# Optimization experiments

Measured on AMD Instinct MI355X. Metric: run time of the kernel, lower is better.

## Reference

```python
import jax, jax.numpy as jnp
import numpy as np

NEG_SLOPE = 0.2

def gat_conv(x, edge_index, W, a_src, a_dst, bias, heads, channels):
    # PyG GATConv (add_self_loops=False, dropout off in eval)
    N = x.shape[0]
    h = (x @ W).reshape(N, heads, channels)               # [N,H,C]
    src, dst = edge_index[0], edge_index[1]
    e_src = jnp.einsum('nhc,hc->nh', h, a_src)            # [N,H]
    e_dst = jnp.einsum('nhc,hc->nh', h, a_dst)
    e = jax.nn.leaky_relu(e_src[src] + e_dst[dst], NEG_SLOPE)  # [E,H]
    # softmax over incoming edges of each destination node
    m = jax.ops.segment_max(e, dst, num_segments=N)       # [N,H]
    ex = jnp.exp(e - m[dst])
    s = jax.ops.segment_sum(ex, dst, num_segments=N)
    alpha = ex / (s[dst] + 1e-16)                         # [E,H]
    msg = h[src] * alpha[:, :, None]                      # [E,H,C]
    out = jax.ops.segment_sum(msg, dst, num_segments=N)   # [N,H,C]
    return out.reshape(N, heads * channels) + bias


def setup_inputs() -> dict:
    key = jax.random.key(0)
    ks = jax.random.split(key, 12)
    N, E, SED, HID, H, F_OUT = 20000, 320000, 768, 128, 4, 128
    return {
        'x': jax.random.normal(ks[0], (N, SED), jnp.float32),
        'edge_index': jax.random.randint(ks[1], (2, E), 0, N, jnp.int32),
        'sentence_embedding': jax.random.normal(ks[2], (SED,), jnp.float32),
        'W1': jax.random.normal(ks[3], (2 * SED, H * HID), jnp.float32) * 0.02,
        'a1_src': jax.random.normal(ks[4], (H, HID), jnp.float32) * 0.1,
        'a1_dst': jax.random.normal(ks[5], (H, HID), jnp.float32) * 0.1,
        'b1': jax.random.normal(ks[6], (H * HID,), jnp.float32) * 0.02,
        'W2': jax.random.normal(ks[7], (H * HID, F_OUT), jnp.float32) * 0.02,
        'a2_src': jax.random.normal(ks[8], (1, F_OUT), jnp.float32) * 0.1,
        'a2_dst': jax.random.normal(ks[9], (1, F_OUT), jnp.float32) * 0.1,
        'b2': jax.random.normal(ks[10], (F_OUT,), jnp.float32) * 0.02,
    }


def reference(x, edge_index, sentence_embedding, W1, a1_src, a1_dst, b1, W2, a2_src, a2_dst, b2):
    N = x.shape[0]
    sent = jnp.broadcast_to(sentence_embedding[None, :], (N, sentence_embedding.shape[0]))
    h = jnp.concatenate([x, sent], axis=1)                # [N, 2*SED]
    h = gat_conv(h, edge_index, W1, a1_src, a1_dst, b1, heads=4, channels=128)
    h = jax.nn.elu(h)
    out = gat_conv(h, edge_index, W2, a2_src, a2_dst, b2, heads=1, channels=128)
    return out
```

## Files before the change

### kernel.cpp

```cpp
#include <hip/hip_runtime.h>
#include <cstdint>
#include <cstddef>

#define NSLOPE 0.2f

typedef __attribute__((ext_vector_type(8))) short bf16x8;
typedef __attribute__((ext_vector_type(4))) float f32x4;
typedef __attribute__((ext_vector_type(2))) float f32x2;
typedef unsigned short ushort_t;

__device__ inline ushort_t f2bf(float f) {
    union { float f; unsigned u; } v; v.f = f;
    unsigned u = v.u;
    unsigned r = (u + 0x7fffu + ((u >> 16) & 1u)) >> 16;
    return (ushort_t)r;
}
__device__ inline float bf2f(ushort_t u) {
    union { unsigned u; float f; } v; v.u = ((unsigned)u) << 16;
    return v.f;
}
__device__ inline float2 unpack_bf2(unsigned u) {
    return make_float2(bf2f((ushort_t)(u & 0xffffu)), bf2f((ushort_t)(u >> 16)));
}
__device__ inline f32x2 unpack2(unsigned u) {
    union { unsigned u; float f; } lo, hi;
    lo.u = u << 16;
    hi.u = u & 0xffff0000u;
    f32x2 r; r.x = lo.f; r.y = hi.f;
    return r;
}
__device__ inline float leaky(float v) { return (v > 0.f) ? v : NSLOPE * v; }
__device__ inline float sel4(float4 q, bool b1, bool b2) {
    return b2 ? (b1 ? q.w : q.z) : (b1 ? q.y : q.x);
}

__global__ __launch_bounds__(256) void prep_kernel(
    const float* __restrict__ x, ushort_t* __restrict__ x_bf16, size_t nx,
    const float* __restrict__ W1, ushort_t* __restrict__ W1T,
    const float* __restrict__ W2, ushort_t* __restrict__ W2T,
    const float* __restrict__ sent, float* __restrict__ svec_part,
    int* __restrict__ indeg, int N, int nbCast, int nbZero)
{
    __shared__ float tile[32][33];
    int bid = blockIdx.x;
    int tid = threadIdx.x;
    if (bid < nbCast) {
        size_t i = ((size_t)bid * 256 + tid) * 8;
        if (i < nx) {
            float4 v0 = *(const float4*)(x + i);
            float4 v1 = *(const float4*)(x + i + 4);
            ushort_t r[8] = { f2bf(v0.x), f2bf(v0.y), f2bf(v0.z), f2bf(v0.w),
                              f2bf(v1.x), f2bf(v1.y), f2bf(v1.z), f2bf(v1.w) };
            *(uint4*)(x_bf16 + i) = *(uint4*)r;
        }
        return;
    }
    bid -= nbCast;
    if (bid < 384) {
        int k0 = (bid % 24) * 32, n0 = (bid / 24) * 32;
        int tx = tid & 31, ty = tid >> 5;
#pragma unroll
        for (int i = 0; i < 4; ++i)
            tile[ty + i * 8][tx] = W1[(size_t)(k0 + ty + i * 8) * 512 + n0 + tx];
        __syncthreads();
#pragma unroll
        for (int i = 0; i < 4; ++i)
            W1T[(size_t)(n0 + ty + i * 8) * 768 + k0 + tx] = f2bf(tile[tx][ty + i * 8]);
        return;
    }
    bid -= 384;
    if (bid < 64) {
        int k0 = (bid % 16) * 32, n0 = (bid / 16) * 32;
        int tx = tid & 31, ty = tid >> 5;
#pragma unroll
        for (int i = 0; i < 4; ++i)
            tile[ty + i * 8][tx] = W2[(size_t)(k0 + ty + i * 8) * 128 + n0 + tx];
        __syncthreads();
#pragma unroll
        for (int i = 0; i < 4; ++i)
            W2T[(size_t)(n0 + ty + i * 8) * 512 + k0 + tx] = f2bf(tile[tx][ty + i * 8]);
        return;
    }
    bid -= 64;
    if (bid < 16) {
        int cb = bid & 1, kb = bid >> 1;
        int c = cb * 256 + tid;
        int k0 = kb * 96;
        float acc = 0.f;
#pragma unroll 8
        for (int k = k0; k < k0 + 96; ++k)
            acc += sent[k] * W1[(size_t)(768 + k) * 512 + c];
        svec_part[kb * 512 + c] = acc;
        return;
    }
    bid -= 16;
    {
        int i = bid * 256 + tid;
        if (i < N) indeg[i] = 0;
    }
}

__device__ inline void async_copy16(const void* g, void* l) {
    __builtin_amdgcn_global_load_lds(
        (const __attribute__((address_space(1))) unsigned int*)g,
        (__attribute__((address_space(3))) unsigned int*)l, 16, 0, 0);
}

__global__ __launch_bounds__(256) void mfma_gemm_kernel(
    const ushort_t* __restrict__ A,
    const ushort_t* __restrict__ BT,
    const float* __restrict__ bias,
    ushort_t* __restrict__ Cb,
    const float* __restrict__ asrc,
    const float* __restrict__ adst,
    float* __restrict__ e_src,
    float* __restrict__ e_dst,
    int eStride,
    int M, int K, int Nc)
{
    __shared__ __align__(16) ushort_t lA[2][128 * 32];
    __shared__ __align__(16) ushort_t lB[2][128 * 32];
    __shared__ float e_lds[128][2][2];
    const int tid = threadIdx.x;
    const int wave = tid >> 6;
    const int lane = tid & 63;
    const int col0 = blockIdx.x * 128;
    const int row0 = blockIdx.y * 128;
    const int wm = (wave & 1) * 64;
    const int wn = (wave >> 1) * 64;
    const int q = lane >> 4;
    const int ml = lane & 15;

    f32x4 acc[4][4] = {};

    int rowS[2], gS[2];
#pragma unroll
    for (int i = 0; i < 2; ++i) {
        int p = wave * 128 + i * 64 + lane;
        int r = p >> 2, s = p & 3;
        rowS[i] = r;
        gS[i] = s ^ ((r >> 1) & 3);
    }

    auto stage = [&](int k0, int buf) {
#pragma unroll
        for (int i = 0; i < 2; ++i) {
            int pb = wave * 128 + i * 64;
            int r = rowS[i];
            int ga = min(row0 + r, M - 1);
            async_copy16(A + (size_t)ga * K + k0 + gS[i] * 8, &lA[buf][(size_t)pb * 8]);
            async_copy16(BT + (size_t)(col0 + r) * K + k0 + gS[i] * 8, &lB[buf][(size_t)pb * 8]);
        }
    };

    stage(0, 0);
    __syncthreads();
    int pb = 0;
    for (int k0 = 0; k0 < K; k0 += 32) {
        if (k0 + 32 < K) stage(k0 + 32, pb ^ 1);
        bf16x8 af[4], bfr[4];
#pragma unroll
        for (int t = 0; t < 4; ++t) {
            int m = wm + t * 16 + ml;
            af[t] = *(const bf16x8*)&lA[pb][(size_t)(m * 4 + (q ^ ((m >> 1) & 3))) * 8];
            int n = wn + t * 16 + ml;
            bfr[t] = *(const bf16x8*)&lB[pb][(size_t)(n * 4 + (q ^ ((n >> 1) & 3))) * 8];
        }
#pragma unroll
        for (int tm = 0; tm < 4; ++tm)
#pragma unroll
            for (int tn = 0; tn < 4; ++tn)
                acc[tm][tn] = __builtin_amdgcn_mfma_f32_16x16x32_bf16(
                    af[tm], bfr[tn], acc[tm][tn], 0, 0, 0);
        __syncthreads();
        pb ^= 1;
    }

    float es_acc[4][4] = {};
    float ed_acc[4][4] = {};
#pragma unroll
    for (int tm = 0; tm < 4; ++tm) {
        int rbase = row0 + wm + tm * 16 + q * 4;
#pragma unroll
        for (int tn = 0; tn < 4; ++tn) {
            int col = col0 + wn + tn * 16 + ml;
            float bb = bias ? bias[col] : 0.f;
            float av = asrc[col];
            float dv = adst[col];
#pragma unroll
            for (int r = 0; r < 4; ++r) {
                int row = rbase + r;
                float val = acc[tm][tn][r] + bb;
                if (row < M)
                    Cb[(size_t)row * Nc + col] = f2bf(val);
                es_acc[tm][r] += val * av;
                ed_acc[tm][r] += val * dv;
            }
        }
    }
    const int colhalf = wave >> 1;
#pragma unroll
    for (int tm = 0; tm < 4; ++tm) {
#pragma unroll
        for (int r = 0; r < 4; ++r) {
            float es = es_acc[tm][r], ed2 = ed_acc[tm][r];
#pragma unroll
            for (int st = 1; st < 16; st <<= 1) {
                es += __shfl_xor(es, st);
                ed2 += __shfl_xor(ed2, st);
            }
            if (ml == 0) {
                int rl = wm + tm * 16 + q * 4 + r;
                e_lds[rl][colhalf][0] = es;
                e_lds[rl][colhalf][1] = ed2;
            }
        }
    }
    __syncthreads();
    if (tid < 128) {
        int row = row0 + tid;
        if (row < M) {
            float es = e_lds[tid][0][0] + e_lds[tid][1][0];
            float ed2 = e_lds[tid][0][1] + e_lds[tid][1][1];
            e_src[(size_t)row * eStride + blockIdx.x] = es;
            e_dst[(size_t)row * eStride + blockIdx.x] = ed2;
        }
    }
}

__global__ void count_kernel(const int* __restrict__ ei, int* __restrict__ indeg, int E) {
    int e = blockIdx.x * blockDim.x + threadIdx.x;
    if (e < E) atomicAdd(&indeg[ei[E + e]], 1);
}

__global__ __launch_bounds__(1024) void scan_kernel(const int* __restrict__ indeg,
                                                    int* __restrict__ offsets,
                                                    int* __restrict__ cursor,
                                                    const float* __restrict__ svec_part,
                                                    float* __restrict__ svec, int N) {
    __shared__ int partial[1024];
    int tid = threadIdx.x;
    if (tid < 512) {
        float s = 0.f;
#pragma unroll
        for (int kb = 0; kb < 8; ++kb) s += svec_part[kb * 512 + tid];
        svec[tid] = s;
    }
    int per = (N + 1023) / 1024;
    int start = tid * per;
    int end = min(start + per, N);
    int sum = 0;
    if (start + per <= N && (per & 3) == 0) {
        for (int i = 0; i < per; i += 4) {
            int4 v = *(const int4*)(indeg + start + i);
            sum += v.x + v.y + v.z + v.w;
        }
    } else {
        for (int i = start; i < end; ++i) sum += indeg[i];
    }
    partial[tid] = sum;
    __syncthreads();
    for (int st = 1; st < 1024; st <<= 1) {
        int v = (tid >= st) ? partial[tid - st] : 0;
        __syncthreads();
        partial[tid] += v;
        __syncthreads();
    }
    int run = (tid == 0) ? 0 : partial[tid - 1];
    if (start + per <= N && (per & 3) == 0) {
        for (int i = 0; i < per; i += 4) {
            int4 v = *(const int4*)(indeg + start + i);
            int4 o;
            o.x = run;
            o.y = o.x + v.x;
            o.z = o.y + v.y;
            o.w = o.z + v.z;
            run = o.w + v.w;
            *(int4*)(offsets + start + i) = o;
            *(int4*)(cursor + start + i) = o;
        }
    } else {
        for (int i = start; i < end; ++i) {
            offsets[i] = run; cursor[i] = run;
            run += indeg[i];
        }
    }
    if (tid == 1023) offsets[N] = run;
}

__global__ void scatter_kernel(const int* __restrict__ ei, int* __restrict__ cursor,
                               int* __restrict__ csr_src, int E) {
    int e = blockIdx.x * blockDim.x + threadIdx.x;
    if (e < E) {
        int d = ei[E + e];
        int p = atomicAdd(&cursor[d], 1);
        csr_src[p] = ei[e];
    }
}

__global__ __launch_bounds__(256) void gather1_kernel(
    const ushort_t* __restrict__ h1b, const float* __restrict__ e_src,
    const float* __restrict__ e_dst, const int* __restrict__ offsets,
    const int* __restrict__ csr_src, const float* __restrict__ bias,
    ushort_t* __restrict__ outb, int N)
{
    int node = __builtin_amdgcn_readfirstlane(blockIdx.x * 4 + (threadIdx.x >> 6));
    int lane = threadIdx.x & 63;
    if (node >= N) return;
    int beg = offsets[node], end = offsets[node + 1];
    float4 ed = *(const float4*)&e_dst[node * 4];

    float m[4] = { -1e30f, -1e30f, -1e30f, -1e30f };
    float s[4] = { 0.f, 0.f, 0.f, 0.f };
    for (int j = beg + lane; j < end; j += 64) {
        int sid = csr_src[j];
        float4 es = *(const float4*)&e_src[sid * 4];
        float e[4] = { leaky(es.x + ed.x), leaky(es.y + ed.y),
                       leaky(es.z + ed.z), leaky(es.w + ed.w) };
#pragma unroll
        for (int hh = 0; hh < 4; ++hh) {
            float nm = fmaxf(m[hh], e[hh]);
            s[hh] = s[hh] * __expf(m[hh] - nm) + __expf(e[hh] - nm);
            m[hh] = nm;
        }
    }
#pragma unroll
    for (int st = 32; st >= 1; st >>= 1) {
#pragma unroll
        for (int hh = 0; hh < 4; ++hh) {
            float om = __shfl_xor(m[hh], st);
            float os = __shfl_xor(s[hh], st);
            float nm = fmaxf(m[hh], om);
            s[hh] = s[hh] * __expf(m[hh] - nm) + os * __expf(om - nm);
            m[hh] = nm;
        }
    }
    const int h = lane >> 4;
    const bool b1 = (h & 1), b2 = (h & 2);
    float mh  = b2 ? (b1 ? m[3] : m[2]) : (b1 ? m[1] : m[0]);
    float sh  = b2 ? (b1 ? s[3] : s[2]) : (b1 ? s[1] : s[0]);
    float rsh = 1.f / (sh + 1e-16f);
    float edh = sel4(ed, b1, b2);

    const ushort_t* hp = h1b + lane * 8;
    f32x2 acc[4] = {};
    int j = beg;
#pragma unroll 2
    for (; j + 4 <= end; j += 4) {
        int s0 = csr_src[j], s1 = csr_src[j + 1];
        int s2 = csr_src[j + 2], s3 = csr_src[j + 3];
        float4 q0 = *(const float4*)&e_src[s0 * 4];
        float4 q1 = *(const float4*)&e_src[s1 * 4];
        float4 q2 = *(const float4*)&e_src[s2 * 4];
        float4 q3 = *(const float4*)&e_src[s3 * 4];
        float w0 = __expf(leaky(sel4(q0, b1, b2) + edh) - mh) * rsh;
        float w1 = __expf(leaky(sel4(q1, b1, b2) + edh) - mh) * rsh;
        float w2 = __expf(leaky(sel4(q2, b1, b2) + edh) - mh) * rsh;
        float w3 = __expf(leaky(sel4(q3, b1, b2) + edh) - mh) * rsh;
        uint4 u0 = *(const uint4*)&hp[(size_t)s0 * 512];
        uint4 u1 = *(const uint4*)&hp[(size_t)s1 * 512];
        uint4 u2 = *(const uint4*)&hp[(size_t)s2 * 512];
        uint4 u3 = *(const uint4*)&hp[(size_t)s3 * 512];
        f32x2 wv;
        wv.x = w0; wv.y = w0;
        acc[0] += unpack2(u0.x) * wv; acc[1] += unpack2(u0.y) * wv;
        acc[2] += unpack2(u0.z) * wv; acc[3] += unpack2(u0.w) * wv;
        wv.x = w1; wv.y = w1;
        acc[0] += unpack2(u1.x) * wv; acc[1] += unpack2(u1.y) * wv;
        acc[2] += unpack2(u1.z) * wv; acc[3] += unpack2(u1.w) * wv;
        wv.x = w2; wv.y = w2;
        acc[0] += unpack2(u2.x) * wv; acc[1] += unpack2(u2.y) * wv;
        acc[2] += unpack2(u2.z) * wv; acc[3] += unpack2(u2.w) * wv;
        wv.x = w3; wv.y = w3;
        acc[0] += unpack2(u3.x) * wv; acc[1] += unpack2(u3.y) * wv;
        acc[2] += unpack2(u3.z) * wv; acc[3] += unpack2(u3.w) * wv;
    }
    for (; j < end; ++j) {
        int s0 = csr_src[j];
        float4 q0 = *(const float4*)&e_src[s0 * 4];
        float w0 = __expf(leaky(sel4(q0, b1, b2) + edh) - mh) * rsh;
        uint4 u0 = *(const uint4*)&hp[(size_t)s0 * 512];
        f32x2 wv; wv.x = w0; wv.y = w0;
        acc[0] += unpack2(u0.x) * wv; acc[1] += unpack2(u0.y) * wv;
        acc[2] += unpack2(u0.z) * wv; acc[3] += unpack2(u0.w) * wv;
    }
    int c = lane * 8;
    ushort_t o[8];
#pragma unroll
    for (int i = 0; i < 4; ++i) {
        float r0 = acc[i].x + bias[c + 2 * i];
        float r1 = acc[i].y + bias[c + 2 * i + 1];
        r0 = (r0 > 0.f) ? r0 : (__expf(r0) - 1.f);
        r1 = (r1 > 0.f) ? r1 : (__expf(r1) - 1.f);
        o[2 * i] = f2bf(r0);
        o[2 * i + 1] = f2bf(r1);
    }
    *(uint4*)&outb[(size_t)node * 512 + c] = *(uint4*)o;
}

__global__ __launch_bounds__(256) void gather2_kernel(
    const ushort_t* __restrict__ h2b, const float* __restrict__ e_src,
    const float* __restrict__ e_dst, const int* __restrict__ offsets,
    const int* __restrict__ csr_src, const float* __restrict__ bias,
    float* __restrict__ out, int N)
{
    int node = __builtin_amdgcn_readfirstlane(blockIdx.x * 4 + (threadIdx.x >> 6));
    int lane = threadIdx.x & 63;
    if (node >= N) return;
    int beg = offsets[node], end = offsets[node + 1];
    float ed = e_dst[node];

    float m = -1e30f, s = 0.f;
    for (int j = beg + lane; j < end; j += 64) {
        float e = leaky(e_src[csr_src[j]] + ed);
        float nm = fmaxf(m, e);
        s = s * __expf(m - nm) + __expf(e - nm);
        m = nm;
    }
#pragma unroll
    for (int st = 32; st >= 1; st >>= 1) {
        float om = __shfl_xor(m, st);
        float os = __shfl_xor(s, st);
        float nm = fmaxf(m, om);
        s = s * __expf(m - nm) + os * __expf(om - nm);
        m = nm;
    }
    float rs = 1.f / (s + 1e-16f);

    const ushort_t* hp = h2b + lane * 2;
    f32x2 acc = { 0.f, 0.f };
    int j = beg;
#pragma unroll 2
    for (; j + 4 <= end; j += 4) {
        int s0 = csr_src[j], s1 = csr_src[j + 1];
        int s2 = csr_src[j + 2], s3 = csr_src[j + 3];
        float w0 = __expf(leaky(e_src[s0] + ed) - m) * rs;
        float w1 = __expf(leaky(e_src[s1] + ed) - m) * rs;
        float w2 = __expf(leaky(e_src[s2] + ed) - m) * rs;
        float w3 = __expf(leaky(e_src[s3] + ed) - m) * rs;
        unsigned u0 = *(const unsigned*)&hp[(size_t)s0 * 128];
        unsigned u1 = *(const unsigned*)&hp[(size_t)s1 * 128];
        unsigned u2 = *(const unsigned*)&hp[(size_t)s2 * 128];
        unsigned u3 = *(const unsigned*)&hp[(size_t)s3 * 128];
        f32x2 w0v = { w0, w0 }, w1v = { w1, w1 }, w2v = { w2, w2 }, w3v = { w3, w3 };
        acc += unpack2(u0) * w0v;
        acc += unpack2(u1) * w1v;
        acc += unpack2(u2) * w2v;
        acc += unpack2(u3) * w3v;
    }
    for (; j < end; ++j) {
        int s0 = csr_src[j];
        float w0 = __expf(leaky(e_src[s0] + ed) - m) * rs;
        unsigned u0 = *(const unsigned*)&hp[(size_t)s0 * 128];
        f32x2 w0v = { w0, w0 };
        acc += unpack2(u0) * w0v;
    }
    float2 o = make_float2(acc.x + bias[lane * 2], acc.y + bias[lane * 2 + 1]);
    *(float2*)&out[(size_t)node * 128 + lane * 2] = o;
}

extern "C" void kernel_launch(void* const* d_in, const int* in_sizes, int n_in,
                              void* d_out, int out_size, void* d_ws, size_t ws_size,
                              hipStream_t stream) {
    const float* x      = (const float*)d_in[0];
    const int*   ei     = (const int*)  d_in[1];
    const float* sent   = (const float*)d_in[2];
    const float* W1     = (const float*)d_in[3];
    const float* a1_src = (const float*)d_in[4];
    const float* a1_dst = (const float*)d_in[5];
    const float* b1     = (const float*)d_in[6];
    const float* W2     = (const float*)d_in[7];
    const float* a2_src = (const float*)d_in[8];
    const float* a2_dst = (const float*)d_in[9];
    const float* b2     = (const float*)d_in[10];
    float* out = (float*)d_out;

    const int N = in_sizes[0] / 768;
    const int E = in_sizes[1] / 2;

    char* p = (char*)d_ws;
    auto carve = [&](size_t bytes) {
        char* q = p;
        p += (bytes + 255) & ~(size_t)255;
        return q;
    };
    ushort_t* h1b = (ushort_t*)carve((size_t)N * 512 * 2);
    char* shared_region = carve((size_t)N * 768 * 2);
    ushort_t* x_bf16 = (ushort_t*)shared_region;
    ushort_t* h_elu_b = (ushort_t*)shared_region;
    ushort_t* h2b = (ushort_t*)carve((size_t)N * 128 * 2);
    ushort_t* W1T = (ushort_t*)carve((size_t)512 * 768 * 2);
    ushort_t* W2T = (ushort_t*)carve((size_t)128 * 512 * 2);
    float* svec_part = (float*)carve(8 * 512 * 4);
    float* svec   = (float*)carve(512 * 4);
    float* e_src1 = (float*)carve((size_t)N * 4 * 4);
    float* e_dst1 = (float*)carve((size_t)N * 4 * 4);
    float* e_src2 = (float*)carve((size_t)N * 4);
    float* e_dst2 = (float*)carve((size_t)N * 4);
    int*   indeg  = (int*)carve((size_t)N * 4);
    int*   offs   = (int*)carve((size_t)(N + 1) * 4);
    int*   cursor = (int*)carve((size_t)N * 4);
    int*   csrsrc = (int*)carve((size_t)E * 4);

    size_t nx = (size_t)N * 768;
    int nbCast = (int)((nx / 8 + 255) / 256);
    int nbZero = (N + 255) / 256;
    int nbPrep = nbCast + 384 + 64 + 16 + nbZero;

    prep_kernel<<<nbPrep, 256, 0, stream>>>(x, x_bf16, nx, W1, W1T, W2, W2T,
                                            sent, svec_part, indeg, N, nbCast, nbZero);
    count_kernel<<<(E + 255) / 256, 256, 0, stream>>>(ei, indeg, E);
    scan_kernel<<<1, 1024, 0, stream>>>(indeg, offs, cursor, svec_part, svec, N);
    scatter_kernel<<<(E + 255) / 256, 256, 0, stream>>>(ei, cursor, csrsrc, E);

    mfma_gemm_kernel<<<dim3(4, (N + 127) / 128), 256, 0, stream>>>(
        x_bf16, W1T, svec, h1b, a1_src, a1_dst, e_src1, e_dst1, 4, N, 768, 512);

    gather1_kernel<<<(N + 3) / 4, 256, 0, stream>>>(
        h1b, e_src1, e_dst1, offs, csrsrc, b1, h_elu_b, N);

    mfma_gemm_kernel<<<dim3(1, (N + 127) / 128), 256, 0, stream>>>(
        h_elu_b, W2T, nullptr, h2b, a2_src, a2_dst, e_src2, e_dst2, 1, N, 512, 128);

    gather2_kernel<<<(N + 3) / 4, 256, 0, stream>>>(
        h2b, e_src2, e_dst2, offs, csrsrc, b2, out, N);
}
```

Before: 295.8 us.

## Triple-buffer GEMM K-loop with vmcnt waits and XCD-aware block remapping

The MFMA GEMM moves from double to triple LDS buffering and prefetches two K-tiles ahead. Full __syncthreads calls are replaced with explicit s_waitcnt vmcnt/lgkmcnt plus s_barrier, so one stage of loads can stay in flight while the current tile is consumed. Block indices are also remapped so that blocks on the same XCD share row tiles, which should improve L2 reuse of A. The row grid is padded to a multiple of 8; the extra blocks do clamped, discarded work. LDS use grows, which may lower occupancy.

Result: no change. 295.7 us (-0.0%).

```diff
diff --git a/kernel.cpp b/kernel.cpp
--- a/kernel.cpp
+++ b/kernel.cpp
@@ -118,14 +118,21 @@
     int eStride,
     int M, int K, int Nc)
 {
-    __shared__ __align__(16) ushort_t lA[2][128 * 32];
-    __shared__ __align__(16) ushort_t lB[2][128 * 32];
+    __shared__ __align__(16) ushort_t lA[3][128 * 32];
+    __shared__ __align__(16) ushort_t lB[3][128 * 32];
     __shared__ float e_lds[128][2][2];
     const int tid = threadIdx.x;
     const int wave = tid >> 6;
     const int lane = tid & 63;
-    const int col0 = blockIdx.x * 128;
-    const int row0 = blockIdx.y * 128;
+
+    const int h = blockIdx.y * gridDim.x + blockIdx.x;
+    const int xcd = h & 7;
+    const int slot = h >> 3;
+    const int by = xcd + 8 * (slot / gridDim.x);
+    const int bx = slot % gridDim.x;
+
+    const int col0 = bx * 128;
+    const int row0 = by * 128;
     const int wm = (wave & 1) * 64;
     const int wn = (wave >> 1) * 64;
     const int q = lane >> 4;
@@ -153,18 +160,25 @@
         }
     };
 
+    const int nt = K >> 5;
     stage(0, 0);
-    __syncthreads();
-    int pb = 0;
-    for (int k0 = 0; k0 < K; k0 += 32) {
-        if (k0 + 32 < K) stage(k0 + 32, pb ^ 1);
+    if (nt > 1) {
+        stage(32, 1);
+        asm volatile("s_waitcnt vmcnt(4)\n\ts_barrier" ::: "memory");
+    } else {
+        asm volatile("s_waitcnt vmcnt(0)\n\ts_barrier" ::: "memory");
+    }
+
+    for (int t = 0; t < nt; ++t) {
+        const int pb = t % 3;
+        if (t + 2 < nt) stage((t + 2) << 5, (t + 2) % 3);
         bf16x8 af[4], bfr[4];
 #pragma unroll
-        for (int t = 0; t < 4; ++t) {
-            int m = wm + t * 16 + ml;
-            af[t] = *(const bf16x8*)&lA[pb][(size_t)(m * 4 + (q ^ ((m >> 1) & 3))) * 8];
-            int n = wn + t * 16 + ml;
-            bfr[t] = *(const bf16x8*)&lB[pb][(size_t)(n * 4 + (q ^ ((n >> 1) & 3))) * 8];
+        for (int tt = 0; tt < 4; ++tt) {
+            int m = wm + tt * 16 + ml;
+            af[tt] = *(const bf16x8*)&lA[pb][(size_t)(m * 4 + (q ^ ((m >> 1) & 3))) * 8];
+            int n = wn + tt * 16 + ml;
+            bfr[tt] = *(const bf16x8*)&lB[pb][(size_t)(n * 4 + (q ^ ((n >> 1) & 3))) * 8];
         }
 #pragma unroll
         for (int tm = 0; tm < 4; ++tm)
@@ -172,8 +186,10 @@
             for (int tn = 0; tn < 4; ++tn)
                 acc[tm][tn] = __builtin_amdgcn_mfma_f32_16x16x32_bf16(
                     af[tm], bfr[tn], acc[tm][tn], 0, 0, 0);
-        __syncthreads();
-        pb ^= 1;
+        if (t + 2 < nt)
+            asm volatile("s_waitcnt vmcnt(4) lgkmcnt(0)\n\ts_barrier" ::: "memory");
+        else if (t + 1 < nt)
+            asm volatile("s_waitcnt vmcnt(0) lgkmcnt(0)\n\ts_barrier" ::: "memory");
     }
 
     float es_acc[4][4] = {};
@@ -222,8 +238,8 @@
         if (row < M) {
             float es = e_lds[tid][0][0] + e_lds[tid][1][0];
             float ed2 = e_lds[tid][0][1] + e_lds[tid][1][1];
-            e_src[(size_t)row * eStride + blockIdx.x] = es;
-            e_dst[(size_t)row * eStride + blockIdx.x] = ed2;
+            e_src[(size_t)row * eStride + bx] = es;
+            e_dst[(size_t)row * eStride + bx] = ed2;
         }
     }
 }
@@ -513,13 +529,15 @@
     scan_kernel<<<1, 1024, 0, stream>>>(indeg, offs, cursor, svec_part, svec, N);
     scatter_kernel<<<(E + 255) / 256, 256, 0, stream>>>(ei, cursor, csrsrc, E);
 
-    mfma_gemm_kernel<<<dim3(4, (N + 127) / 128), 256, 0, stream>>>(
+    int nyPad = (((N + 127) / 128) + 7) & ~7;
+
+    mfma_gemm_kernel<<<dim3(4, nyPad), 256, 0, stream>>>(
         x_bf16, W1T, svec, h1b, a1_src, a1_dst, e_src1, e_dst1, 4, N, 768, 512);
 
     gather1_kernel<<<(N + 3) / 4, 256, 0, stream>>>(
         h1b, e_src1, e_dst1, offs, csrsrc, b1, h_elu_b, N);
 
-    mfma_gemm_kernel<<<dim3(1, (N + 127) / 128), 256, 0, stream>>>(
+    mfma_gemm_kernel<<<dim3(1, nyPad), 256, 0, stream>>>(
         h_elu_b, W2T, nullptr, h2b, a2_src, a2_dst, e_src2, e_dst2, 1, N, 512, 128);
 
     gather2_kernel<<<(N + 3) / 4, 256, 0, stream>>>(
```
